# Performance work log

Measured on AMD Instinct MI355X. Metric: run time of the kernel, lower is better.

Reference implementation:

```python
import jax, jax.numpy as jnp
import numpy as np

N = 100000   # nodes
E = 1600000  # edges
D_IN = 7
H1 = 64
H2 = 32
G = 64       # graphs in batch


def setup_inputs() -> dict:
    key = jax.random.key(0)
    ks = jax.random.split(key, 10)
    x = jax.random.normal(ks[0], (N, D_IN), jnp.float32)
    edge_index = jax.random.randint(ks[1], (2, E), 0, N, dtype=jnp.int64)
    batch = jnp.sort(jax.random.randint(ks[2], (N,), 0, G, dtype=jnp.int64))
    # Glorot-style init for GCN weights
    W1 = jax.random.normal(ks[3], (D_IN, H1), jnp.float32) * (1.0 / np.sqrt(D_IN))
    b1 = jnp.zeros((H1,), jnp.float32)
    W2 = jax.random.normal(ks[4], (H1, H2), jnp.float32) * (1.0 / np.sqrt(H1))
    b2 = jnp.zeros((H2,), jnp.float32)
    W3 = jax.random.normal(ks[5], (H1, H2), jnp.float32) * (1.0 / np.sqrt(H1))
    b3 = jnp.zeros((H2,), jnp.float32)
    eps = jax.random.normal(ks[6], (N, H2), jnp.float32)  # reparam noise
    return dict(x=x, edge_index=edge_index, batch=batch,
                W1=W1, b1=b1, W2=W2, b2=b2, W3=W3, b3=b3, eps=eps)


def _gcn_agg(xw, src, dst, dis):
    # Symmetric-normalized aggregation with self-loops (PyG GCNConv default):
    # out[i] = sum_{(j->i)} d_i^{-1/2} d_j^{-1/2} xw[j] + d_i^{-1} xw[i]
    norm = (dis[src] * dis[dst])[:, None]
    msg = xw[src] * norm                      # [E, H] gather
    out = jax.ops.segment_sum(msg, dst, num_segments=N)  # scatter-add
    return out + xw * (dis * dis)[:, None]    # self-loop term


def reference(x, edge_index, batch, W1, b1, W2, b2, W3, b3, eps):
    src, dst = edge_index[0], edge_index[1]
    # degree on A + I (targets), unit edge weights
    deg = jax.ops.segment_sum(jnp.ones((E,), x.dtype), dst, num_segments=N) + 1.0
    dis = jax.lax.rsqrt(deg)  # deg^{-1/2}

    hidden1 = jax.nn.relu(_gcn_agg(x @ W1, src, dst, dis) + b1)

    # global mean pool of raw x over graphs
    counts = jax.ops.segment_sum(jnp.ones((N,), x.dtype), batch, num_segments=G)
    x_pooled = jax.ops.segment_sum(x, batch, num_segments=G) / jnp.maximum(counts, 1.0)[:, None]

    mu = jax.nn.relu(_gcn_agg(hidden1 @ W2, src, dst, dis) + b2)
    logvar = jax.nn.relu(_gcn_agg(hidden1 @ W3, src, dst, dis) + b3)

    # reparameterize: std = exp(logvar) (no 0.5 factor, as in source)
    z = eps * jnp.exp(logvar) + mu
    return z, x_pooled, mu, logvar
```

## Files before the change

kernel.cpp:

```cpp
#include <hip/hip_runtime.h>
#include <hip/hip_bf16.h>
#include <hip/hip_fp16.h>

#define NN 100000
#define NE 1600000
#define D_IN 7
#define H1 64
#define H2 32
#define NG 64
#define TE 2048
#define NTILE 782
#define BSH 9
#define NBUK 196
#define CAP 10240

typedef _Float16 f16x8 __attribute__((ext_vector_type(8)));
typedef float f32x4 __attribute__((ext_vector_type(4)));

__device__ int lower_bound_i(const int* a, int n, int v) {
    int lo = 0, hi = n;
    while (lo < hi) { int mid = (lo + hi) >> 1; if (a[mid] < v) lo = mid + 1; else hi = mid; }
    return lo;
}

__global__ void k_pi(const float* __restrict__ x, const int* __restrict__ batch,
                     float* __restrict__ outp, int* __restrict__ bucket_cursor) {
    int g = blockIdx.x, t = threadIdx.x;
    if (g == NG) {
        if (t < 256) bucket_cursor[t] = t * CAP;
        return;
    }
    __shared__ int bounds[2];
    __shared__ float red[256 * D_IN];
    if (t == 0) {
        bounds[0] = lower_bound_i(batch, NN, g);
        bounds[1] = lower_bound_i(batch, NN, g + 1);
    }
    __syncthreads();
    int s = bounds[0], e = bounds[1];
    float acc[D_IN];
#pragma unroll
    for (int k = 0; k < D_IN; k++) acc[k] = 0.f;
    for (int n = s + t; n < e; n += 256) {
#pragma unroll
        for (int k = 0; k < D_IN; k++) acc[k] += x[n * D_IN + k];
    }
#pragma unroll
    for (int k = 0; k < D_IN; k++) red[t * D_IN + k] = acc[k];
    __syncthreads();
    if (t < D_IN) {
        float sum = 0.f;
        for (int i = 0; i < 256; i++) sum += red[i * D_IN + t];
        float cnt = (float)(e - s);
        outp[g * D_IN + t] = sum / fmaxf(cnt, 1.f);
    }
}

__global__ __launch_bounds__(256) void k_bin(const int* __restrict__ src,
                                             const int* __restrict__ dst,
                                             int* __restrict__ bucket_cursor,
                                             int* __restrict__ staging) {
    __shared__ int hist[NBUK];
    __shared__ int startx[NBUK];
    __shared__ int runb[NBUK];
    __shared__ int cur[NBUK];
    __shared__ int wsum[4];
    __shared__ int2 pairs[TE];
    int t = threadIdx.x;
    int base = blockIdx.x * TE;
    int tile_cnt = min(TE, NE - base);
    for (int i = t; i < NBUK; i += 256) hist[i] = 0;
    __syncthreads();
    int myd[TE / 256], mys[TE / 256];
#pragma unroll
    for (int k = 0; k < TE / 256; k++) {
        int i = base + k * 256 + t;
        if (i < NE) {
            myd[k] = dst[i]; mys[k] = src[i];
            atomicAdd(&hist[myd[k] >> BSH], 1);
        } else myd[k] = -1;
    }
    __syncthreads();
    int hv = (t < NBUK) ? hist[t] : 0;
    int lane = t & 63, wv = t >> 6;
    int sv = hv;
#pragma unroll
    for (int off = 1; off < 64; off <<= 1) {
        int n = __shfl_up(sv, off, 64);
        if (lane >= off) sv += n;
    }
    if (lane == 63) wsum[wv] = sv;
    __syncthreads();
    int wbase = 0;
#pragma unroll
    for (int i = 0; i < 4; i++) wbase += (i < wv) ? wsum[i] : 0;
    if (t < NBUK) {
        int ex = wbase + sv - hv;
        startx[t] = ex;
        cur[t] = ex;
        if (hv > 0) runb[t] = atomicAdd(&bucket_cursor[t], hv);
    }
    __syncthreads();
#pragma unroll
    for (int k = 0; k < TE / 256; k++) {
        if (myd[k] >= 0) {
            int b = myd[k] >> BSH;
            int slot = atomicAdd(&cur[b], 1);
            pairs[slot] = make_int2(myd[k], mys[k]);
        }
    }
    __syncthreads();
    for (int i = t; i < tile_cnt; i += 256) {
        int2 p = pairs[i];
        int b = p.x >> BSH;
        staging[runb[b] + (i - startx[b])] = ((p.x & 511) << 17) | p.y;
    }
}

__global__ __launch_bounds__(512) void k_build(const int* __restrict__ staging,
                                               const int* __restrict__ bucket_cursor,
                                               int2* __restrict__ rowinfo,
                                               float* __restrict__ dis,
                                               int* __restrict__ csr,
                                               const float* __restrict__ x,
                                               float* __restrict__ xd8) {
    __shared__ int cnt[512];
    __shared__ int cur[512];
    __shared__ int wsum[8];
    int t = threadIdx.x;
    int nbase = blockIdx.x << BSH;
    int ebase = blockIdx.x * CAP;
    int eend = bucket_cursor[blockIdx.x];
    cnt[t] = 0;
    __syncthreads();
    for (int i = ebase + t; i < eend; i += 512)
        atomicAdd(&cnt[staging[i] >> 17], 1);
    __syncthreads();
    int v = cnt[t];
    int lane = t & 63, wv = t >> 6;
    int sv = v;
#pragma unroll
    for (int off = 1; off < 64; off <<= 1) {
        int n = __shfl_up(sv, off, 64);
        if (lane >= off) sv += n;
    }
    if (lane == 63) wsum[wv] = sv;
    __syncthreads();
    int wbase = 0;
#pragma unroll
    for (int i = 0; i < 8; i++) wbase += (i < wv) ? wsum[i] : 0;
    int excl = wbase + sv - v;
    cur[t] = excl;
    int node = nbase + t;
    if (node < NN) {
        rowinfo[node] = make_int2(ebase + excl, v);
        float d = rsqrtf((float)v + 1.0f);
        dis[node] = d;
        const float* xr = x + (size_t)node * D_IN;
        float4 w0 = make_float4(d * xr[0], d * xr[1], d * xr[2], d * xr[3]);
        float4 w1 = make_float4(d * xr[4], d * xr[5], d * xr[6], 0.f);
        float4* xo = (float4*)(xd8 + (size_t)node * 8);
        xo[0] = w0; xo[1] = w1;
    }
    __syncthreads();
    for (int i = ebase + t; i < eend; i += 512) {
        int p = staging[i];
        int pos = ebase + atomicAdd(&cur[p >> 17], 1);
        csr[pos] = p & 0x1FFFF;
    }
}

__global__ __launch_bounds__(256) void k_aggx(const int2* __restrict__ rowinfo,
                                              const float* __restrict__ dis,
                                              const int* __restrict__ csr,
                                              const float* __restrict__ xd8,
                                              const float* __restrict__ W1,
                                              const float* __restrict__ b1,
                                              __half* __restrict__ h1h) {
    __shared__ float sW[D_IN * H1];
    __shared__ float sb[H1];
    __shared__ float sAx[64 * 9];
    int t = threadIdx.x;
    for (int i = t; i < D_IN * H1; i += 256) sW[i] = W1[i];
    if (t < H1) sb[t] = b1[t];
    int ll = t & 3;
    int ln = t >> 2;
    int node = blockIdx.x * 64 + ln;
    int nodec = min(node, NN - 1);
    int2 ri = rowinfo[nodec];
    int start = ri.x, c = ri.y;
    int cpos = start + max(c - 1, 0);
    int cmax = c;
    cmax = max(cmax, __shfl_xor(cmax, 4, 64));
    cmax = max(cmax, __shfl_xor(cmax, 8, 64));
    cmax = max(cmax, __shfl_xor(cmax, 16, 64));
    cmax = max(cmax, __shfl_xor(cmax, 32, 64));
    const float2* xb = (const float2*)xd8;
    float2 acc[4];
#pragma unroll
    for (int k = 0; k < 4; k++) acc[k] = make_float2(0.f, 0.f);
    for (int j = 0; j < cmax; j += 8) {
#pragma unroll
        for (int k = 0; k < 8; k++) {
            bool v = (j + k) < c;
            int s = csr[min(start + j + k, cpos)];
            s = v ? s : nodec;
            float2 r = xb[(size_t)s * 4 + ll];
            acc[k & 3].x += v ? r.x : 0.f;
            acc[k & 3].y += v ? r.y : 0.f;
        }
    }
    float sx = acc[0].x + acc[1].x + acc[2].x + acc[3].x;
    float sy = acc[0].y + acc[1].y + acc[2].y + acc[3].y;
    float2 self = xb[(size_t)nodec * 4 + ll];
    float dn = dis[nodec];
    sAx[ln * 9 + 2 * ll]     = dn * (sx + self.x);
    sAx[ln * 9 + 2 * ll + 1] = dn * (sy + self.y);
    __syncthreads();
    if (node < NN) {
        const float* axp = &sAx[ln * 9];
        union { __half h[16]; float4 f[2]; } u;
#pragma unroll
        for (int j = 0; j < 16; j++) {
            int h = ll * 16 + j;
            float a = sb[h];
#pragma unroll
            for (int k = 0; k < D_IN; k++) a += axp[k] * sW[k * H1 + h];
            u.h[j] = __float2half(dn * fmaxf(a, 0.f));
        }
        float4* d4 = (float4*)(h1h + (size_t)node * H1 + ll * 16);
        d4[0] = u.f[0];
        d4[1] = u.f[1];
    }
}

__device__ __forceinline__ float4 h4_to_f4(float2 r) {
    __half2 h0 = *reinterpret_cast<__half2*>(&r.x);
    __half2 h1 = *reinterpret_cast<__half2*>(&r.y);
    float2 f0 = __half22float2(h0);
    float2 f1 = __half22float2(h1);
    return make_float4(f0.x, f0.y, f1.x, f1.y);
}

__device__ __forceinline__ void pk_acc_m(__half2& p, __half2& q, float2 r, bool v) {
    unsigned ux = v ? *reinterpret_cast<unsigned*>(&r.x) : 0u;
    unsigned uy = v ? *reinterpret_cast<unsigned*>(&r.y) : 0u;
    p = __hadd2(p, *reinterpret_cast<__half2*>(&ux));
    q = __hadd2(q, *reinterpret_cast<__half2*>(&uy));
}

__global__ __launch_bounds__(256) void k_agg2f(const int2* __restrict__ rowinfo,
                                               const float* __restrict__ dis,
                                               const int* __restrict__ csr,
                                               const __half* __restrict__ h1h,
                                               const float* __restrict__ W2,
                                               const float* __restrict__ W3,
                                               const float* __restrict__ b2,
                                               const float* __restrict__ b3,
                                               const float* __restrict__ eps,
                                               float* __restrict__ out_z,
                                               float* __restrict__ out_mu,
                                               float* __restrict__ out_lv) {
    __shared__ __align__(16) _Float16 sW[64 * 80];
    __shared__ __align__(16) _Float16 sT[64 * 72];
    int t = threadIdx.x;
    for (int i = t; i < 64 * 64; i += 256) {
        int c = i >> 6, k = i & 63;
        float w = (c < 32) ? W2[k * H2 + c] : W3[k * H2 + (c - 32)];
        sW[c * 80 + k] = (_Float16)w;
    }
    int lane = t & 63;
    int wv = t >> 6;
    int sub = lane >> 4, l15 = lane & 15;
    const float2* yb = (const float2*)h1h;
    for (int g = 0; g < 4; g++) {
        int lrow = wv * 16 + g * 4 + sub;
        int node = blockIdx.x * 64 + lrow;
        int nodec = min(node, NN - 1);
        int2 ri = rowinfo[nodec];
        int start = ri.x, c = ri.y;
        int cpos = start + max(c - 1, 0);
        int cmax = c;
        cmax = max(cmax, __shfl_xor(cmax, 16, 64));
        cmax = max(cmax, __shfl_xor(cmax, 32, 64));
        __half2 z2 = __float2half2_rn(0.f);
        __half2 p[4] = {z2, z2, z2, z2};
        __half2 q[4] = {z2, z2, z2, z2};
        for (int j = 0; j < cmax; j += 8) {
#pragma unroll
            for (int k = 0; k < 8; k++) {
                bool v = (j + k) < c;
                int s = csr[min(start + j + k, cpos)];
                s = v ? s : nodec;
                float2 r = yb[(size_t)s * 16 + l15];
                pk_acc_m(p[k & 3], q[k & 3], r, v);
            }
        }
        __half2 sp = __hadd2(__hadd2(p[0], p[1]), __hadd2(p[2], p[3]));
        __half2 sq = __hadd2(__hadd2(q[0], q[1]), __hadd2(q[2], q[3]));
        float2 fp = __half22float2(sp), fq = __half22float2(sq);
        float4 sv = h4_to_f4(yb[(size_t)nodec * 16 + l15]);
        float dn = dis[nodec];
        __half2 ha, hb;
        ha.x = __float2half(dn * (fp.x + sv.x)); ha.y = __float2half(dn * (fp.y + sv.y));
        hb.x = __float2half(dn * (fq.x + sv.z)); hb.y = __float2half(dn * (fq.y + sv.w));
        float2 st;
        st.x = *reinterpret_cast<float*>(&ha);
        st.y = *reinterpret_cast<float*>(&hb);
        *(float2*)&sT[lrow * 72 + l15 * 4] = st;
    }
    __syncthreads();
    int c15 = l15, k8 = sub;
    const _Float16* ap = &sT[(wv * 16 + c15) * 72];
    f16x8 a0 = *(const f16x8*)(ap + k8 * 8);
    f16x8 a1 = *(const f16x8*)(ap + 32 + k8 * 8);
    const _Float16* wb = sW + (size_t)c15 * 80 + k8 * 8;
    f16x8 b00 = *(const f16x8*)(wb);
    f16x8 b01 = *(const f16x8*)(wb + 32);
    f16x8 b10 = *(const f16x8*)(wb + 16 * 80);
    f16x8 b11 = *(const f16x8*)(wb + 16 * 80 + 32);
    f16x8 b20 = *(const f16x8*)(wb + 32 * 80);
    f16x8 b21 = *(const f16x8*)(wb + 32 * 80 + 32);
    f16x8 b30 = *(const f16x8*)(wb + 48 * 80);
    f16x8 b31 = *(const f16x8*)(wb + 48 * 80 + 32);
    f32x4 ac0 = {0.f, 0.f, 0.f, 0.f};
    f32x4 ac1 = ac0, ac2 = ac0, ac3 = ac0;
    ac0 = __builtin_amdgcn_mfma_f32_16x16x32_f16(a0, b00, ac0, 0, 0, 0);
    ac0 = __builtin_amdgcn_mfma_f32_16x16x32_f16(a1, b01, ac0, 0, 0, 0);
    ac1 = __builtin_amdgcn_mfma_f32_16x16x32_f16(a0, b10, ac1, 0, 0, 0);
    ac1 = __builtin_amdgcn_mfma_f32_16x16x32_f16(a1, b11, ac1, 0, 0, 0);
    ac2 = __builtin_amdgcn_mfma_f32_16x16x32_f16(a0, b20, ac2, 0, 0, 0);
    ac2 = __builtin_amdgcn_mfma_f32_16x16x32_f16(a1, b21, ac2, 0, 0, 0);
    ac3 = __builtin_amdgcn_mfma_f32_16x16x32_f16(a0, b30, ac3, 0, 0, 0);
    ac3 = __builtin_amdgcn_mfma_f32_16x16x32_f16(a1, b31, ac3, 0, 0, 0);
    float bb2a = b2[c15], bb2b = b2[c15 + 16];
    float bb3a = b3[c15], bb3b = b3[c15 + 16];
    int srow = blockIdx.x * 64 + wv * 16 + k8 * 4;
#pragma unroll
    for (int i = 0; i < 4; i++) {
        int r = srow + i;
        if (r < NN) {
            float mu0 = fmaxf(ac0[i] + bb2a, 0.f);
            float mu1 = fmaxf(ac1[i] + bb2b, 0.f);
            float lv0 = fmaxf(ac2[i] + bb3a, 0.f);
            float lv1 = fmaxf(ac3[i] + bb3b, 0.f);
            size_t o0 = (size_t)r * 32 + c15;
            float e0 = eps[o0], e1 = eps[o0 + 16];
            out_mu[o0]      = mu0;
            out_mu[o0 + 16] = mu1;
            out_lv[o0]      = lv0;
            out_lv[o0 + 16] = lv1;
            out_z[o0]       = e0 * __expf(lv0) + mu0;
            out_z[o0 + 16]  = e1 * __expf(lv1) + mu1;
        }
    }
}

extern "C" void kernel_launch(void* const* d_in, const int* in_sizes, int n_in,
                              void* d_out, int out_size, void* d_ws, size_t ws_size,
                              hipStream_t stream) {
    const float* x   = (const float*)d_in[0];
    const int*   ei  = (const int*)d_in[1];
    const int*   bat = (const int*)d_in[2];
    const float* W1  = (const float*)d_in[3];
    const float* b1  = (const float*)d_in[4];
    const float* W2  = (const float*)d_in[5];
    const float* b2  = (const float*)d_in[6];
    const float* W3  = (const float*)d_in[7];
    const float* b3  = (const float*)d_in[8];
    const float* eps = (const float*)d_in[9];

    const int* src = ei;
    const int* dst = ei + NE;

    float* out = (float*)d_out;
    float* out_z    = out;
    float* out_pool = out + (size_t)NN * H2;
    float* out_mu   = out_pool + NG * D_IN;
    float* out_lv   = out_mu + (size_t)NN * H2;

    int*    bucket_cursor = (int*)d_ws;
    int2*   rowinfo       = (int2*)(bucket_cursor + 256);
    float*  dis           = (float*)(rowinfo + NN);
    int*    staging       = (int*)(dis + NN);
    int*    csr           = staging + (size_t)NBUK * CAP;
    __half* h1h           = (__half*)(csr + (size_t)NBUK * CAP);
    float*  xd8           = (float*)(h1h + (size_t)NN * H1);

    k_pi    <<<NG + 1, 256, 0, stream>>>(x, bat, out_pool, bucket_cursor);
    k_bin   <<<NTILE, 256, 0, stream>>>(src, dst, bucket_cursor, staging);
    k_build <<<NBUK, 512, 0, stream>>>(staging, bucket_cursor, rowinfo, dis, csr, x, xd8);
    k_aggx  <<<(NN + 63) / 64, 256, 0, stream>>>(rowinfo, dis, csr, xd8, W1, b1, h1h);
    k_agg2f <<<(NN + 63) / 64, 256, 0, stream>>>(rowinfo, dis, csr, h1h, W2, W3,
                                                 b2, b3, eps, out_z, out_mu, out_lv);
}
```

Before: 210.7 us.

## Batch gather loads in aggregation loops and spread agg2 rows across 16 waves

Both aggregation kernels now load 16 CSR indices first, then issue 16 feature gathers, then accumulate, so more memory loads are in flight per thread. The second aggregation kernel grows from 256 to 1024 threads per block, so each wave handles one group of 4 rows instead of looping over 4 groups. This aims to hide gather latency through higher memory parallelism. In exchange, register pressure rises from the 16-wide arrays, and 12 of the 16 waves sit idle during the MFMA epilogue.

Result: slower. 217.0 us (+3.0%).

```diff
diff --git a/kernel.cpp b/kernel.cpp
--- a/kernel.cpp
+++ b/kernel.cpp
@@ -199,15 +199,21 @@
     float2 acc[4];
 #pragma unroll
     for (int k = 0; k < 4; k++) acc[k] = make_float2(0.f, 0.f);
-    for (int j = 0; j < cmax; j += 8) {
-#pragma unroll
-        for (int k = 0; k < 8; k++) {
+    for (int j = 0; j < cmax; j += 16) {
+        int sarr[16];
+#pragma unroll
+        for (int k = 0; k < 16; k++) {
+            int s = csr[min(start + j + k, cpos)];
+            sarr[k] = ((j + k) < c) ? s : nodec;
+        }
+        float2 r[16];
+#pragma unroll
+        for (int k = 0; k < 16; k++) r[k] = xb[(size_t)sarr[k] * 4 + ll];
+#pragma unroll
+        for (int k = 0; k < 16; k++) {
             bool v = (j + k) < c;
-            int s = csr[min(start + j + k, cpos)];
-            s = v ? s : nodec;
-            float2 r = xb[(size_t)s * 4 + ll];
-            acc[k & 3].x += v ? r.x : 0.f;
-            acc[k & 3].y += v ? r.y : 0.f;
+            acc[k & 3].x += v ? r[k].x : 0.f;
+            acc[k & 3].y += v ? r[k].y : 0.f;
         }
     }
     float sx = acc[0].x + acc[1].x + acc[2].x + acc[3].x;
@@ -249,69 +255,73 @@
     q = __hadd2(q, *reinterpret_cast<__half2*>(&uy));
 }
 
-__global__ __launch_bounds__(256) void k_agg2f(const int2* __restrict__ rowinfo,
-                                               const float* __restrict__ dis,
-                                               const int* __restrict__ csr,
-                                               const __half* __restrict__ h1h,
-                                               const float* __restrict__ W2,
-                                               const float* __restrict__ W3,
-                                               const float* __restrict__ b2,
-                                               const float* __restrict__ b3,
-                                               const float* __restrict__ eps,
-                                               float* __restrict__ out_z,
-                                               float* __restrict__ out_mu,
-                                               float* __restrict__ out_lv) {
+__global__ __launch_bounds__(1024) void k_agg2f(const int2* __restrict__ rowinfo,
+                                                const float* __restrict__ dis,
+                                                const int* __restrict__ csr,
+                                                const __half* __restrict__ h1h,
+                                                const float* __restrict__ W2,
+                                                const float* __restrict__ W3,
+                                                const float* __restrict__ b2,
+                                                const float* __restrict__ b3,
+                                                const float* __restrict__ eps,
+                                                float* __restrict__ out_z,
+                                                float* __restrict__ out_mu,
+                                                float* __restrict__ out_lv) {
     __shared__ __align__(16) _Float16 sW[64 * 80];
     __shared__ __align__(16) _Float16 sT[64 * 72];
     int t = threadIdx.x;
-    for (int i = t; i < 64 * 64; i += 256) {
+    for (int i = t; i < 64 * 64; i += 1024) {
         int c = i >> 6, k = i & 63;
         float w = (c < 32) ? W2[k * H2 + c] : W3[k * H2 + (c - 32)];
         sW[c * 80 + k] = (_Float16)w;
     }
     int lane = t & 63;
-    int wv = t >> 6;
+    int w = t >> 6;
     int sub = lane >> 4, l15 = lane & 15;
     const float2* yb = (const float2*)h1h;
-    for (int g = 0; g < 4; g++) {
-        int lrow = wv * 16 + g * 4 + sub;
-        int node = blockIdx.x * 64 + lrow;
-        int nodec = min(node, NN - 1);
-        int2 ri = rowinfo[nodec];
-        int start = ri.x, c = ri.y;
-        int cpos = start + max(c - 1, 0);
-        int cmax = c;
-        cmax = max(cmax, __shfl_xor(cmax, 16, 64));
-        cmax = max(cmax, __shfl_xor(cmax, 32, 64));
-        __half2 z2 = __float2half2_rn(0.f);
-        __half2 p[4] = {z2, z2, z2, z2};
-        __half2 q[4] = {z2, z2, z2, z2};
-        for (int j = 0; j < cmax; j += 8) {
-#pragma unroll
-            for (int k = 0; k < 8; k++) {
-                bool v = (j + k) < c;
-                int s = csr[min(start + j + k, cpos)];
-                s = v ? s : nodec;
-                float2 r = yb[(size_t)s * 16 + l15];
-                pk_acc_m(p[k & 3], q[k & 3], r, v);
-            }
-        }
-        __half2 sp = __hadd2(__hadd2(p[0], p[1]), __hadd2(p[2], p[3]));
-        __half2 sq = __hadd2(__hadd2(q[0], q[1]), __hadd2(q[2], q[3]));
-        float2 fp = __half22float2(sp), fq = __half22float2(sq);
-        float4 sv = h4_to_f4(yb[(size_t)nodec * 16 + l15]);
-        float dn = dis[nodec];
-        __half2 ha, hb;
-        ha.x = __float2half(dn * (fp.x + sv.x)); ha.y = __float2half(dn * (fp.y + sv.y));
-        hb.x = __float2half(dn * (fq.x + sv.z)); hb.y = __float2half(dn * (fq.y + sv.w));
-        float2 st;
-        st.x = *reinterpret_cast<float*>(&ha);
-        st.y = *reinterpret_cast<float*>(&hb);
-        *(float2*)&sT[lrow * 72 + l15 * 4] = st;
-    }
-    __syncthreads();
+    int lrow = w * 4 + sub;
+    int node = blockIdx.x * 64 + lrow;
+    int nodec = min(node, NN - 1);
+    int2 ri = rowinfo[nodec];
+    int start = ri.x, c = ri.y;
+    int cpos = start + max(c - 1, 0);
+    int cmax = c;
+    cmax = max(cmax, __shfl_xor(cmax, 16, 64));
+    cmax = max(cmax, __shfl_xor(cmax, 32, 64));
+    __half2 z2 = __float2half2_rn(0.f);
+    __half2 p[4] = {z2, z2, z2, z2};
+    __half2 q[4] = {z2, z2, z2, z2};
+    for (int j = 0; j < cmax; j += 16) {
+        int sarr[16];
+#pragma unroll
+        for (int k = 0; k < 16; k++) {
+            int s = csr[min(start + j + k, cpos)];
+            sarr[k] = ((j + k) < c) ? s : nodec;
+        }
+        float2 r[16];
+#pragma unroll
+        for (int k = 0; k < 16; k++)
+            r[k] = yb[(size_t)sarr[k] * 16 + l15];
+#pragma unroll
+        for (int k = 0; k < 16; k++)
+            pk_acc_m(p[k & 3], q[k & 3], r[k], (j + k) < c);
+    }
+    __half2 sp = __hadd2(__hadd2(p[0], p[1]), __hadd2(p[2], p[3]));
+    __half2 sq = __hadd2(__hadd2(q[0], q[1]), __hadd2(q[2], q[3]));
+    float2 fp = __half22float2(sp), fq = __half22float2(sq);
+    float4 sv = h4_to_f4(yb[(size_t)nodec * 16 + l15]);
+    float dn = dis[nodec];
+    __half2 ha, hb;
+    ha.x = __float2half(dn * (fp.x + sv.x)); ha.y = __float2half(dn * (fp.y + sv.y));
+    hb.x = __float2half(dn * (fq.x + sv.z)); hb.y = __float2half(dn * (fq.y + sv.w));
+    float2 st;
+    st.x = *reinterpret_cast<float*>(&ha);
+    st.y = *reinterpret_cast<float*>(&hb);
+    *(float2*)&sT[lrow * 72 + l15 * 4] = st;
+    __syncthreads();
+    if (w >= 4) return;
     int c15 = l15, k8 = sub;
-    const _Float16* ap = &sT[(wv * 16 + c15) * 72];
+    const _Float16* ap = &sT[(w * 16 + c15) * 72];
     f16x8 a0 = *(const f16x8*)(ap + k8 * 8);
     f16x8 a1 = *(const f16x8*)(ap + 32 + k8 * 8);
     const _Float16* wb = sW + (size_t)c15 * 80 + k8 * 8;
@@ -335,7 +345,7 @@
     ac3 = __builtin_amdgcn_mfma_f32_16x16x32_f16(a1, b31, ac3, 0, 0, 0);
     float bb2a = b2[c15], bb2b = b2[c15 + 16];
     float bb3a = b3[c15], bb3b = b3[c15 + 16];
-    int srow = blockIdx.x * 64 + wv * 16 + k8 * 4;
+    int srow = blockIdx.x * 64 + w * 16 + k8 * 4;
 #pragma unroll
     for (int i = 0; i < 4; i++) {
         int r = srow + i;
@@ -391,6 +401,6 @@
     k_bin   <<<NTILE, 256, 0, stream>>>(src, dst, bucket_cursor, staging);
     k_build <<<NBUK, 512, 0, stream>>>(staging, bucket_cursor, rowinfo, dis, csr, x, xd8);
     k_aggx  <<<(NN + 63) / 64, 256, 0, stream>>>(rowinfo, dis, csr, xd8, W1, b1, h1h);
-    k_agg2f <<<(NN + 63) / 64, 256, 0, stream>>>(rowinfo, dis, csr, h1h, W2, W3,
-                                                 b2, b3, eps, out_z, out_mu, out_lv);
-}
+    k_agg2f <<<(NN + 63) / 64, 1024, 0, stream>>>(rowinfo, dis, csr, h1h, W2, W3,
+                                                  b2, b3, eps, out_z, out_mu, out_lv);
+}
```
